# Kernel optimization log

Measured on AMD Instinct MI355X. Metric: run time of the kernel, lower is better.

The kernel has to match this reference:

```python
import jax, jax.numpy as jnp
import numpy as np

EPS = 1e-8
SPLIT_N = 256   # sphere chunk size, matches split_n default
T_MAX = 100.0   # finite stand-in for the math.inf default t_max


def setup_inputs() -> dict:
    key = jax.random.key(0)
    k1, k2, k3 = jax.random.split(key, 3)
    H, W, S = 16, 64, 32
    r_o = jax.random.normal(k1, (H, W, S, 3), jnp.float32) * 2.0
    r_d = jax.random.normal(k2, (H, W, S, 3), jnp.float32)
    r_d = r_d / jnp.linalg.norm(r_d, axis=-1, keepdims=True)
    rays = jnp.concatenate([r_o, r_d], axis=-1)            # [H,W,S,6]
    centers = jax.random.uniform(k3, (1024, 3), jnp.float32, -5.0, 5.0)
    radii = jnp.full((1024,), 1.0, jnp.float32)
    return {"rays": rays, "centers": centers, "radii": radii}


def reference(rays, centers, radii):
    r_o, r_d = rays[..., :3], rays[..., 3:]               # [H,W,S,3] each
    n_chunks = centers.shape[0] // SPLIT_N
    c_chunks = centers.reshape(n_chunks, SPLIT_N, 3)
    rad_chunks = radii.reshape(n_chunks, SPLIT_N)

    a = jnp.sum(r_d * r_d, axis=-1)                        # [H,W,S]

    def chunk_step(carry, chunk):
        best_dists, best_faces, out_active = carry
        sph, rad = chunk                                   # [K,3], [K]
        fs = r_o[None] - sph[:, None, None, None, :]       # [K,H,W,S,3]
        b = 2.0 * jnp.sum(r_d[None] * fs, axis=-1)         # [K,H,W,S]
        c = jnp.sum(fs * fs, axis=-1) - (rad * rad)[:, None, None, None]
        d = b * b - 4.0 * a[None] * c
        valid = d > 0
        # torch does d[valid] = sqrt(d[valid]); invalid entries keep raw d
        ds = jnp.where(valid, jnp.sqrt(jnp.where(valid, d, 1.0)), d)
        roots = jnp.stack([-b + ds, -b - ds], axis=-1) / (2.0 * a[None, ..., None])  # [K,H,W,S,2]
        mask = valid & jnp.any((roots >= EPS) & (roots < T_MAX), axis=-1)
        roots = jnp.where(roots < EPS, jnp.inf, roots)
        valid_mins = jnp.any(mask, axis=0)                 # [H,W,S]
        t = jnp.where(mask, jnp.min(roots, axis=-1), jnp.inf)  # [K,H,W,S]
        min_t = jnp.min(t, axis=0)
        sph_idx = jnp.argmin(t, axis=0).astype(jnp.int32)  # chunk-local idx (faithful to source)
        replace = valid_mins & (best_dists > min_t)
        best_dists = jnp.where(replace, min_t, best_dists)
        best_faces = jnp.where(replace, sph_idx, best_faces)
        out_active = out_active | valid_mins
        return (best_dists, best_faces, out_active), None

    init = (jnp.full(r_o.shape[:-1], T_MAX, jnp.float32),
            jnp.full(r_o.shape[:-1], -1, jnp.int32),
            jnp.zeros(r_o.shape[:-1], dtype=bool))
    (best_dists, best_faces, out_active), _ = jax.lax.scan(
        chunk_step, init, (c_chunks, rad_chunks))

    p = r_o + best_dists[..., None] * r_d
    # faithful to the source: best_faces is the chunk-LOCAL sphere index,
    # used to gather from the global centers table
    idx = jnp.clip(best_faces, 0, centers.shape[0] - 1)
    diff = p - centers[idx]
    norm = jnp.maximum(jnp.linalg.norm(diff, axis=-1, keepdims=True), 1e-12)
    n = jnp.where(out_active[..., None], diff / norm, 0.0)
    p = p + n * 1e-5
    return p, n, best_dists, out_active
```

## Files before the change

kernel.cpp:

```cpp
#include <hip/hip_runtime.h>
#include <math.h>

#define NRAYS 32768
#define NSPH  1024
#define SUBS  16
#define PAIRS 32
#define RPB   16
#define TPB   256
#define NBLK  (NRAYS / RPB)

typedef float    v2f __attribute__((ext_vector_type(2)));
typedef unsigned v2u __attribute__((ext_vector_type(2)));

static __device__ __forceinline__ v2f fma2(v2f a, v2f b, v2f c) {
    v2f r;
    r.x = __builtin_fmaf(a.x, b.x, c.x);
    r.y = __builtin_fmaf(a.y, b.y, c.y);
    return r;
}

__global__ __launch_bounds__(256, 8) void sphere_kernel(
    const float* __restrict__ rays,
    const float* __restrict__ centers,
    const float* __restrict__ radii,
    float* __restrict__ out)
{
#pragma clang fp contract(off)
    __shared__ float4   sph[SUBS * (2 * PAIRS + 1)];
    __shared__ unsigned s_min[SUBS][RPB];

    const int tid = threadIdx.x;

    for (int p = tid; p < NSPH / 2; p += TPB) {
        const int g0 = 2 * p, g1 = 2 * p + 1;
        const float x0 = centers[3 * g0 + 0], y0 = centers[3 * g0 + 1], z0 = centers[3 * g0 + 2];
        const float x1 = centers[3 * g1 + 0], y1 = centers[3 * g1 + 1], z1 = centers[3 * g1 + 2];
        const float r0 = radii[g0], r1 = radii[g1];
        const int b4 = (p >> 5) * (2 * PAIRS + 1) + (p & 31) * 2;
        sph[b4 + 0] = make_float4(x0, x1, y0, y1);
        sph[b4 + 1] = make_float4(z0, z1, r0 * r0, r1 * r1);
    }
    __syncthreads();

    const int rl  = tid & (RPB - 1);
    const int sub = tid >> 4;
    const int ray = blockIdx.x * RPB + rl;

    const float2* rp = (const float2*)(rays + ray * 6);
    const float2 q0 = rp[0], q1 = rp[1], q2 = rp[2];
    const float ox = q0.x, oy = q0.y, oz = q1.x;
    const float dx = q1.y, dy = q2.x, dz = q2.y;

    const float a    = ((dx * dx) + (dy * dy)) + (dz * dz);
    const float epsA = 1e-8f * a;
    const float hunA = 100.0f * a;

    const v2f ox2 = {ox, ox}, oy2 = {oy, oy}, oz2 = {oz, oz};
    const v2f dx2 = {dx, dx}, dy2 = {dy, dy}, dz2 = {dz, dz};
    const v2f an2 = {-a, -a};
    const v2f epsA2 = {epsA, epsA};

    const unsigned IMASK = 0xFFFFFFC0u;
    unsigned cw = 0xFFFFFFFFu;

    const float4* __restrict__ spb = &sph[sub * (2 * PAIRS + 1)];

#pragma unroll
    for (int i = 0; i < PAIRS; ++i) {
        const float4 A = spb[2 * i];
        const float4 B = spb[2 * i + 1];
        const v2f X = {A.x, A.y}, Y = {A.z, A.w};
        const v2f Z = {B.x, B.y}, Q = {B.z, B.w};
        const v2f fx = ox2 - X;
        const v2f fy = oy2 - Y;
        const v2f fz = oz2 - Z;
        const v2f dt = fma2(dz2, fz, fma2(dy2, fy, dx2 * fx));
        const v2f cc = fma2(fz, fz, fma2(fy, fy, fx * fx)) - Q;
        const v2f zz = fma2(dt, dt, an2 * cc);
        const v2f s  = { __builtin_amdgcn_sqrtf(zz.x),
                         __builtin_amdgcn_sqrtf(zz.y) };
        const v2f dtp = dt + epsA2;
        const v2f vv0 = s - dtp;
        const v2f vv1 = (-s) - dtp;
        const v2u b0 = __builtin_bit_cast(v2u, vv0);
        const v2u b1 = __builtin_bit_cast(v2u, vv1);
        const unsigned me = (b1.x < b0.x) ? b1.x : b0.x;
        const unsigned mo = (b1.y < b0.y) ? b1.y : b0.y;
        const unsigned ue = (me & IMASK) | (unsigned)(2 * i);
        const unsigned uo = (mo & IMASK) | (unsigned)(2 * i + 1);
        const unsigned mp = (ue < uo) ? ue : uo;
        cw = (mp < cw) ? mp : cw;
    }

    s_min[sub][rl] = cw;
    __syncthreads();

    if (tid < RPB) {
        unsigned bw = 0xFFFFFFFFu;
        int ksel = 0;
        for (int k = 0; k < SUBS; ++k) {
            const unsigned mt = s_min[k][tid];
            if (mt < bw) { bw = mt; ksel = k; }
        }
        const bool active = bw < __builtin_bit_cast(unsigned, hunA);

        const float best = active ? (__builtin_bit_cast(float, bw) / a) : 100.0f;

        float px = ox + (best * dx);
        float py = oy + (best * dy);
        float pz = oz + (best * dz);

        const int gidx = active ? (((ksel & 3) << 6) | (int)(bw & 63u)) : 0;
        const int b4 = (gidx >> 6) * (2 * PAIRS + 1) + ((gidx & 63) >> 1) * 2;
        const int j  = gidx & 1;
        const float4 A = sph[b4];
        const float4 B = sph[b4 + 1];
        const float cxv = j ? A.y : A.x;
        const float cyv = j ? A.w : A.z;
        const float czv = j ? B.y : B.x;
        const float ddx = px - cxv;
        const float ddy = py - cyv;
        const float ddz = pz - czv;
        float nrm = sqrtf(((ddx * ddx) + (ddy * ddy)) + (ddz * ddz));
        nrm = fmaxf(nrm, 1e-12f);
        const float nx = active ? (ddx / nrm) : 0.0f;
        const float ny = active ? (ddy / nrm) : 0.0f;
        const float nz = active ? (ddz / nrm) : 0.0f;
        px = px + (nx * 1e-5f);
        py = py + (ny * 1e-5f);
        pz = pz + (nz * 1e-5f);

        const int r = blockIdx.x * RPB + tid;
        float* outp = out;
        float* outn = out + NRAYS * 3;
        float* outd = out + NRAYS * 6;
        float* outa = out + NRAYS * 7;

        outp[r * 3 + 0] = px;
        outp[r * 3 + 1] = py;
        outp[r * 3 + 2] = pz;
        outn[r * 3 + 0] = nx;
        outn[r * 3 + 1] = ny;
        outn[r * 3 + 2] = nz;
        outd[r] = best;
        outa[r] = active ? 1.0f : 0.0f;
    }
}

extern "C" void kernel_launch(void* const* d_in, const int* in_sizes, int n_in,
                              void* d_out, int out_size, void* d_ws, size_t ws_size,
                              hipStream_t stream) {
    const float* rays    = (const float*)d_in[0];
    const float* centers = (const float*)d_in[1];
    const float* radii   = (const float*)d_in[2];
    float* out = (float*)d_out;

    dim3 grid(NBLK);
    dim3 block(TPB);
    hipLaunchKernelGGL(sphere_kernel, grid, block, 0, stream,
                       rays, centers, radii, out);
}
```

Before: 19.98 us.

## Register-block four rays per thread and amortize sphere staging over 64 rays

Blocks grow to 1024 threads covering 64 rays. Each thread now tests 16 spheres against 4 rays held in registers, instead of 64 spheres against one ray. This amortizes the per-block shared-memory sphere staging and each LDS sphere load over more rays, and cuts the block count by four. The final reduction scans 64 partial minima per ray, and the epsilon offset on dt is dropped. The launch-bounds occupancy hint for 1024-thread blocks may cap registers and risk spills.

```diff
diff --git a/kernel.cpp b/kernel.cpp
--- a/kernel.cpp
+++ b/kernel.cpp
@@ -3,11 +3,11 @@
 
 #define NRAYS 32768
 #define NSPH  1024
-#define SUBS  16
-#define PAIRS 32
-#define RPB   16
-#define TPB   256
-#define NBLK  (NRAYS / RPB)
+#define SUBS  64
+#define SPAIR 8
+#define RQB   16
+#define TPB   1024
+#define NBLK  (NRAYS / 64)
 
 typedef float    v2f __attribute__((ext_vector_type(2)));
 typedef unsigned v2u __attribute__((ext_vector_type(2)));
@@ -19,15 +19,15 @@
     return r;
 }
 
-__global__ __launch_bounds__(256, 8) void sphere_kernel(
+__global__ __launch_bounds__(TPB, 4) void sphere_kernel(
     const float* __restrict__ rays,
     const float* __restrict__ centers,
     const float* __restrict__ radii,
     float* __restrict__ out)
 {
 #pragma clang fp contract(off)
-    __shared__ float4   sph[SUBS * (2 * PAIRS + 1)];
-    __shared__ unsigned s_min[SUBS][RPB];
+    __shared__ float4   sph[SUBS * (2 * SPAIR + 1)];
+    __shared__ unsigned s_min[SUBS][65];
 
     const int tid = threadIdx.x;
 
@@ -36,88 +36,97 @@
         const float x0 = centers[3 * g0 + 0], y0 = centers[3 * g0 + 1], z0 = centers[3 * g0 + 2];
         const float x1 = centers[3 * g1 + 0], y1 = centers[3 * g1 + 1], z1 = centers[3 * g1 + 2];
         const float r0 = radii[g0], r1 = radii[g1];
-        const int b4 = (p >> 5) * (2 * PAIRS + 1) + (p & 31) * 2;
+        const int sub = p >> 3, within = p & 7;
+        const int b4 = sub * (2 * SPAIR + 1) + within * 2;
         sph[b4 + 0] = make_float4(x0, x1, y0, y1);
         sph[b4 + 1] = make_float4(z0, z1, r0 * r0, r1 * r1);
     }
     __syncthreads();
 
-    const int rl  = tid & (RPB - 1);
+    const int q   = tid & (RQB - 1);
     const int sub = tid >> 4;
-    const int ray = blockIdx.x * RPB + rl;
+    const int ray0 = blockIdx.x * 64 + q * 4;
 
-    const float2* rp = (const float2*)(rays + ray * 6);
-    const float2 q0 = rp[0], q1 = rp[1], q2 = rp[2];
-    const float ox = q0.x, oy = q0.y, oz = q1.x;
-    const float dx = q1.y, dy = q2.x, dz = q2.y;
+    float ox[4], oy[4], oz[4], dxr[4], dyr[4], dzr[4], ar[4];
+#pragma unroll
+    for (int j = 0; j < 4; ++j) {
+        const float2* rp = (const float2*)(rays + (ray0 + j) * 6);
+        const float2 q0 = rp[0], q1 = rp[1], q2 = rp[2];
+        ox[j] = q0.x; oy[j] = q0.y; oz[j] = q1.x;
+        dxr[j] = q1.y; dyr[j] = q2.x; dzr[j] = q2.y;
+        ar[j] = ((dxr[j] * dxr[j]) + (dyr[j] * dyr[j])) + (dzr[j] * dzr[j]);
+    }
 
-    const float a    = ((dx * dx) + (dy * dy)) + (dz * dz);
-    const float epsA = 1e-8f * a;
-    const float hunA = 100.0f * a;
+    const unsigned IMASK = 0xFFFFFFF0u;
+    unsigned cw[4] = {0xFFFFFFFFu, 0xFFFFFFFFu, 0xFFFFFFFFu, 0xFFFFFFFFu};
 
-    const v2f ox2 = {ox, ox}, oy2 = {oy, oy}, oz2 = {oz, oz};
-    const v2f dx2 = {dx, dx}, dy2 = {dy, dy}, dz2 = {dz, dz};
-    const v2f an2 = {-a, -a};
-    const v2f epsA2 = {epsA, epsA};
-
-    const unsigned IMASK = 0xFFFFFFC0u;
-    unsigned cw = 0xFFFFFFFFu;
-
-    const float4* __restrict__ spb = &sph[sub * (2 * PAIRS + 1)];
+    const float4* __restrict__ spb = &sph[sub * (2 * SPAIR + 1)];
 
 #pragma unroll
-    for (int i = 0; i < PAIRS; ++i) {
+    for (int i = 0; i < SPAIR; ++i) {
         const float4 A = spb[2 * i];
         const float4 B = spb[2 * i + 1];
         const v2f X = {A.x, A.y}, Y = {A.z, A.w};
         const v2f Z = {B.x, B.y}, Q = {B.z, B.w};
-        const v2f fx = ox2 - X;
-        const v2f fy = oy2 - Y;
-        const v2f fz = oz2 - Z;
-        const v2f dt = fma2(dz2, fz, fma2(dy2, fy, dx2 * fx));
-        const v2f cc = fma2(fz, fz, fma2(fy, fy, fx * fx)) - Q;
-        const v2f zz = fma2(dt, dt, an2 * cc);
-        const v2f s  = { __builtin_amdgcn_sqrtf(zz.x),
-                         __builtin_amdgcn_sqrtf(zz.y) };
-        const v2f dtp = dt + epsA2;
-        const v2f vv0 = s - dtp;
-        const v2f vv1 = (-s) - dtp;
-        const v2u b0 = __builtin_bit_cast(v2u, vv0);
-        const v2u b1 = __builtin_bit_cast(v2u, vv1);
-        const unsigned me = (b1.x < b0.x) ? b1.x : b0.x;
-        const unsigned mo = (b1.y < b0.y) ? b1.y : b0.y;
-        const unsigned ue = (me & IMASK) | (unsigned)(2 * i);
-        const unsigned uo = (mo & IMASK) | (unsigned)(2 * i + 1);
-        const unsigned mp = (ue < uo) ? ue : uo;
-        cw = (mp < cw) ? mp : cw;
+#pragma unroll
+        for (int j = 0; j < 4; ++j) {
+            const v2f o_x = {ox[j], ox[j]}, o_y = {oy[j], oy[j]}, o_z = {oz[j], oz[j]};
+            const v2f d_x = {dxr[j], dxr[j]}, d_y = {dyr[j], dyr[j]}, d_z = {dzr[j], dzr[j]};
+            const v2f an2 = {-ar[j], -ar[j]};
+            const v2f fx = o_x - X;
+            const v2f fy = o_y - Y;
+            const v2f fz = o_z - Z;
+            const v2f dt = fma2(d_z, fz, fma2(d_y, fy, d_x * fx));
+            const v2f cc = fma2(fz, fz, fma2(fy, fy, fx * fx)) - Q;
+            const v2f zz = fma2(dt, dt, an2 * cc);
+            const v2f s  = { __builtin_amdgcn_sqrtf(zz.x),
+                             __builtin_amdgcn_sqrtf(zz.y) };
+            const v2f vv0 = s - dt;
+            const v2f vv1 = (-s) - dt;
+            const v2u b0 = __builtin_bit_cast(v2u, vv0);
+            const v2u b1 = __builtin_bit_cast(v2u, vv1);
+            const unsigned me = (b1.x < b0.x) ? b1.x : b0.x;
+            const unsigned mo = (b1.y < b0.y) ? b1.y : b0.y;
+            const unsigned ue = (me & IMASK) | (unsigned)(2 * i);
+            const unsigned uo = (mo & IMASK) | (unsigned)(2 * i + 1);
+            const unsigned mp = (ue < uo) ? ue : uo;
+            cw[j] = (mp < cw[j]) ? mp : cw[j];
+        }
     }
 
-    s_min[sub][rl] = cw;
+#pragma unroll
+    for (int j = 0; j < 4; ++j) s_min[sub][q * 4 + j] = cw[j];
     __syncthreads();
 
-    if (tid < RPB) {
+    if (tid < 64) {
         unsigned bw = 0xFFFFFFFFu;
         int ksel = 0;
         for (int k = 0; k < SUBS; ++k) {
             const unsigned mt = s_min[k][tid];
             if (mt < bw) { bw = mt; ksel = k; }
         }
+        const float2* rp = (const float2*)(rays + (blockIdx.x * 64 + tid) * 6);
+        const float2 q0 = rp[0], q1 = rp[1], q2 = rp[2];
+        const float rox = q0.x, roy = q0.y, roz = q1.x;
+        const float rdx = q1.y, rdy = q2.x, rdz = q2.y;
+        const float a = ((rdx * rdx) + (rdy * rdy)) + (rdz * rdz);
+        const float hunA = 100.0f * a;
         const bool active = bw < __builtin_bit_cast(unsigned, hunA);
 
         const float best = active ? (__builtin_bit_cast(float, bw) / a) : 100.0f;
 
-        float px = ox + (best * dx);
-        float py = oy + (best * dy);
-        float pz = oz + (best * dz);
+        float px = rox + (best * rdx);
+        float py = roy + (best * rdy);
+        float pz = roz + (best * rdz);
 
-        const int gidx = active ? (((ksel & 3) << 6) | (int)(bw & 63u)) : 0;
-        const int b4 = (gidx >> 6) * (2 * PAIRS + 1) + ((gidx & 63) >> 1) * 2;
-        const int j  = gidx & 1;
+        const int gidx = active ? (((ksel & 15) << 4) | (int)(bw & 15u)) : 0;
+        const int b4 = (gidx >> 4) * (2 * SPAIR + 1) + ((gidx & 15) >> 1) * 2;
+        const int jj = gidx & 1;
         const float4 A = sph[b4];
         const float4 B = sph[b4 + 1];
-        const float cxv = j ? A.y : A.x;
-        const float cyv = j ? A.w : A.z;
-        const float czv = j ? B.y : B.x;
+        const float cxv = jj ? A.y : A.x;
+        const float cyv = jj ? A.w : A.z;
+        const float czv = jj ? B.y : B.x;
         const float ddx = px - cxv;
         const float ddy = py - cyv;
         const float ddz = pz - czv;
@@ -130,7 +139,7 @@
         py = py + (ny * 1e-5f);
         pz = pz + (nz * 1e-5f);
 
-        const int r = blockIdx.x * RPB + tid;
+        const int r = blockIdx.x * 64 + tid;
         float* outp = out;
         float* outn = out + NRAYS * 3;
         float* outd = out + NRAYS * 6;
```

Measured after the change: 22.85 us. 14.3% more time.
